# Kernel tuning notes

Measured on AMD Instinct MI355X. Metric: run time of the kernel, lower is better.

Reference implementation:

```python
import jax, jax.numpy as jnp
import numpy as np

B, N, F_IN, D, K, INTER = 64, 512, 128, 128, 32, 256
EPS = 1e-5


def _bn(x, g, b, axes):
    # BatchNorm in training mode (biased batch statistics), matching torch BN forward
    m = x.mean(axis=axes, keepdims=True)
    v = x.var(axis=axes, keepdims=True)
    return (x - m) * jax.lax.rsqrt(v + EPS) * g + b


def setup_inputs() -> dict:
    key = jax.random.key(0)
    ks = jax.random.split(key, 12)
    u = lambda k, s: jax.random.uniform(k, s, jnp.float32, -0.3, 0.3)
    return {
        "data": jax.random.normal(ks[0], (B, N, F_IN), jnp.float32),
        "emb_weight": u(ks[1], (N, D)),          # nn.Embedding(node_num, dim), kaiming-uniform-ish
        "lin_W": u(ks[2], (F_IN, D)),            # GraphLayer lin (no bias)
        "att_i": u(ks[3], (D,)),
        "att_j": u(ks[4], (D,)),
        "att_em_i": u(ks[5], (D,)),
        "att_em_j": u(ks[6], (D,)),
        "gnn_bias": jnp.zeros((D,), jnp.float32),
        "gnn_bn_g": jnp.ones((D,), jnp.float32),
        "gnn_bn_b": jnp.zeros((D,), jnp.float32),
        "bn_out_g": jnp.ones((D,), jnp.float32),
        "bn_out_b": jnp.zeros((D,), jnp.float32),
        "W1": u(ks[7], (D, INTER)), "b1": jnp.zeros((INTER,), jnp.float32),
        "bn1_g": jnp.ones((INTER,), jnp.float32), "bn1_b": jnp.zeros((INTER,), jnp.float32),
        "W2": u(ks[8], (INTER, INTER)), "b2": jnp.zeros((INTER,), jnp.float32),
        "bn2_g": jnp.ones((INTER,), jnp.float32), "bn2_b": jnp.zeros((INTER,), jnp.float32),
        "W3": u(ks[9], (INTER, 1)), "b3": jnp.zeros((1,), jnp.float32),
    }


def reference(data, emb_weight, lin_W, att_i, att_j, att_em_i, att_em_j,
              gnn_bias, gnn_bn_g, gnn_bn_b, bn_out_g, bn_out_b,
              W1, b1, bn1_g, bn1_b, W2, b2, bn2_g, bn2_b, W3, b3):
    M = B * N
    x = data.reshape(M, F_IN)

    # --- learned graph: cosine similarity + topk over DETACHED embeddings ---
    w = jax.lax.stop_gradient(emb_weight)
    nrm = jnp.linalg.norm(w, axis=-1)
    cos = (w @ w.T) / (nrm[:, None] * nrm[None, :])
    topk_idx = jax.lax.top_k(cos, K)[1]                    # [N, K]

    # gated_edge_index = (j=topk neighbor as source, i as target), tiled per batch
    src0 = topk_idx.reshape(-1)                            # [N*K] sources (j)
    dst0 = jnp.repeat(jnp.arange(N), K)                    # [N*K] targets (i)
    off = (jnp.arange(B) * N)[:, None]
    src = (src0[None, :] + off).reshape(-1)                # [B*N*K]
    dst = (dst0[None, :] + off).reshape(-1)
    valid = src != dst                                     # remove_self_loops
    loops = jnp.arange(M)                                  # add_self_loops
    src = jnp.concatenate([src, loops])
    dst = jnp.concatenate([dst, loops])
    valid = jnp.concatenate([valid, jnp.ones((M,), bool)])

    # --- GraphLayer (GAT-style, heads=1, concat=False) ---
    x_lin = x @ lin_W                                      # [M, D]
    emb_b = jnp.tile(emb_weight, (B, 1))                   # [M, D] embedding repeated per batch
    # per-node score halves; gather scalars at edges instead of [E, 2D] keys
    s_i = x_lin @ att_i + emb_b @ att_em_i                 # key_i . cat(att_i, att_em_i)
    s_j = x_lin @ att_j + emb_b @ att_em_j
    logit = jax.nn.leaky_relu(s_i[dst] + s_j[src], 0.2)    # [E]
    logit = jnp.where(valid, logit, -1e9)                  # removed self-edges contribute 0
    mx = jax.ops.segment_max(logit, dst, num_segments=M)
    e = jnp.where(valid, jnp.exp(logit - mx[dst]), 0.0)
    den = jax.ops.segment_sum(e, dst, num_segments=M)
    alpha = e / den[dst]                                   # softmax over incoming edges
    agg = jax.ops.segment_sum(x_lin[src] * alpha[:, None], dst, num_segments=M)
    gcn = jax.nn.relu(_bn(agg + gnn_bias, gnn_bn_g, gnn_bn_b, (0,)))  # GNNLayer bn+relu

    # --- gating by embedding, BN over channel dim, OutLayer MLP ---
    h = gcn.reshape(B, N, D) * emb_weight[None]            # [B, N, D]
    h = jax.nn.relu(_bn(h, bn_out_g, bn_out_b, (0, 1)))    # BatchNorm1d over D channels
    # dropout p=0.2 is identity in eval mode
    o = jax.nn.relu(_bn(h @ W1 + b1, bn1_g, bn1_b, (0, 1)))
    o = jax.nn.relu(_bn(o @ W2 + b2, bn2_g, bn2_b, (0, 1)))
    o = (o @ W3 + b3).reshape(B, N)                        # out.view(-1, node_num)
    return o
```

## Files before the change

### kernel.cpp

```cpp
#include <hip/hip_runtime.h>
#include <math.h>

#define M_ROWS 32768
#define NNODES 512
#define KNBR   32
#define EPSBN  1e-5f

typedef __bf16 bf16x8 __attribute__((ext_vector_type(8)));
typedef __bf16 bf16x4 __attribute__((ext_vector_type(4)));
typedef __bf16 bf16x2 __attribute__((ext_vector_type(2)));
typedef float  f32x4  __attribute__((ext_vector_type(4)));

#if defined(__has_builtin)
#if __has_builtin(__builtin_amdgcn_global_load_lds)
#define HAVE_GLL 1
#endif
#endif

__device__ __forceinline__ void async_ld16(void* lds, const void* g){
#ifdef HAVE_GLL
    __builtin_amdgcn_global_load_lds((__attribute__((address_space(1))) void*)(g),
                                     (__attribute__((address_space(3))) void*)(lds),
                                     16, 0, 0);
#else
    *(bf16x8*)lds = *(const bf16x8*)g;
#endif
}

__global__ __launch_bounds__(256) void k1_kernel(
    const float* __restrict__ data, const float* __restrict__ emb,
    const float* __restrict__ lin_W, const float* __restrict__ W1,
    const float* __restrict__ W2,
    const float* __restrict__ att_i, const float* __restrict__ att_j,
    const float* __restrict__ aem_i, const float* __restrict__ aem_j,
    int* __restrict__ topk, float* __restrict__ e_i, float* __restrict__ e_j,
    __bf16* __restrict__ Wp1, __bf16* __restrict__ Wp2,
    float* __restrict__ stats,
    __bf16* __restrict__ xlin, float* __restrict__ s_i, float* __restrict__ s_j)
{
    __shared__ __align__(16) char sm[50176];
    int bid = blockIdx.x, tid = threadIdx.x;

    if (bid < 512){
        __bf16 (*As)[136] = (__bf16(*)[136])sm;
        bf16x8* Bp = (bf16x8*)(sm + 17408);
        int lane = tid & 63, wv = tid >> 6;
        int mrow = lane & 15, q = lane >> 4;
        int row0 = bid * 64;

        #pragma unroll
        for (int i = 0; i < 8; ++i){
            int g = tid + i*256;
            int kg = g >> 7, c = g & 127;
            bf16x8 pk;
            #pragma unroll
            for (int j = 0; j < 8; ++j) pk[j] = (__bf16)lin_W[(size_t)(kg*8 + j)*128 + c];
            Bp[g] = pk;
        }
        #pragma unroll
        for (int i = 0; i < 4; ++i){
            int p = tid + i*256;
            int r = p >> 4, c8 = p & 15;
            const float* src = &data[(size_t)(row0 + r)*128 + c8*8];
            float4 a0 = *(const float4*)src;
            float4 a1 = *(const float4*)(src + 4);
            bf16x8 o;
            o[0]=(__bf16)a0.x; o[1]=(__bf16)a0.y; o[2]=(__bf16)a0.z; o[3]=(__bf16)a0.w;
            o[4]=(__bf16)a1.x; o[5]=(__bf16)a1.y; o[6]=(__bf16)a1.z; o[7]=(__bf16)a1.w;
            *(bf16x8*)&As[r][c8*8] = o;
        }
        __syncthreads();

        f32x4 acc[8];
        #pragma unroll
        for (int ct = 0; ct < 8; ++ct) acc[ct] = (f32x4){0.f,0.f,0.f,0.f};
        #pragma unroll
        for (int ks = 0; ks < 4; ++ks){
            bf16x8 a = *(const bf16x8*)&As[wv*16 + mrow][ks*32 + q*8];
            #pragma unroll
            for (int ct = 0; ct < 8; ++ct){
                bf16x8 bb = Bp[(ks*4 + q)*128 + ct*16 + mrow];
                acc[ct] = __builtin_amdgcn_mfma_f32_16x16x32_bf16(a, bb, acc[ct], 0, 0, 0);
            }
        }

        float ai[4] = {0,0,0,0}, aj[4] = {0,0,0,0};
        #pragma unroll
        for (int ct = 0; ct < 8; ++ct){
            int col = ct*16 + mrow;
            float wti = att_i[col], wtj = att_j[col];
            #pragma unroll
            for (int reg = 0; reg < 4; ++reg){
                int row = row0 + wv*16 + q*4 + reg;
                float v = acc[ct][reg];
                xlin[(size_t)row*128 + col] = (__bf16)v;
                ai[reg] += v*wti; aj[reg] += v*wtj;
            }
        }
        #pragma unroll
        for (int mask = 1; mask < 16; mask <<= 1){
            #pragma unroll
            for (int reg = 0; reg < 4; ++reg){
                ai[reg] += __shfl_xor(ai[reg], mask);
                aj[reg] += __shfl_xor(aj[reg], mask);
            }
        }
        if (mrow == 0){
            #pragma unroll
            for (int reg = 0; reg < 4; ++reg){
                int row = row0 + wv*16 + q*4 + reg;
                s_i[row] = ai[reg];
                s_j[row] = aj[reg];
            }
        }
        return;
    }

    if (bid >= 1024){
        if (bid == 1072){
            for (int i = tid; i < 1536; i += 256) stats[i] = 0.f;
            return;
        }
        int gidx = (bid - 1024)*256 + tid;
        const float* W; __bf16* o; int lg;
        if (gidx < 4096){ W = W1; o = Wp1; lg = gidx; }
        else            { W = W2; o = Wp2; lg = gidx - 4096; }
        int kg = lg >> 8, c = lg & 255;
        bf16x8 pk;
        #pragma unroll
        for (int j = 0; j < 8; ++j) pk[j] = (__bf16)W[(size_t)(kg*8 + j)*256 + c];
        *(bf16x8*)&o[(size_t)lg*8] = pk;
        return;
    }

    float* wi   = (float*)sm;
    float* sval = (float*)(sm + 512);
    int*   sidx = (int*)(sm + 2560);
    int row = bid - 512;
    if (tid < 128) wi[tid] = emb[row*128 + tid];
    __syncthreads();

    if (tid >= 64 && tid < 128){
        int lane = tid - 64;
        float ai = wi[lane]*aem_i[lane] + wi[lane+64]*aem_i[lane+64];
        float aj = wi[lane]*aem_j[lane] + wi[lane+64]*aem_j[lane+64];
        #pragma unroll
        for (int off = 32; off; off >>= 1){
            ai += __shfl_down(ai, off);
            aj += __shfl_down(aj, off);
        }
        if (lane == 0){ e_i[row] = ai; e_j[row] = aj; }
    }

    float ni = 0.f;
    #pragma unroll 8
    for (int d = 0; d < 128; ++d) ni += wi[d]*wi[d];
    float rni = sqrtf(ni);
    for (int jj = tid; jj < 512; jj += 256){
        const float4* wj4 = (const float4*)(emb + jj*128);
        float dot = 0.f, nj = 0.f;
        #pragma unroll 8
        for (int d4 = 0; d4 < 32; ++d4){
            float4 w = wj4[d4];
            dot += wi[4*d4+0]*w.x + wi[4*d4+1]*w.y + wi[4*d4+2]*w.z + wi[4*d4+3]*w.w;
            nj  += w.x*w.x + w.y*w.y + w.z*w.z + w.w*w.w;
        }
        sval[jj] = dot / (rni * sqrtf(nj));
        sidx[jj] = jj;
    }
    __syncthreads();

    #pragma unroll 1
    for (int k = 2; k <= 512; k <<= 1){
        #pragma unroll 1
        for (int j = k >> 1; j > 0; j >>= 1){
            int i2 = ((tid & ~(j-1)) << 1) | (tid & (j-1));
            int p  = i2 | j;
            float vi = sval[i2], vp = sval[p];
            int   xi = sidx[i2], xp = sidx[p];
            bool i_before_p = (vi > vp) || (vi == vp && xi < xp);
            bool up = ((i2 & k) == 0);
            if (up ? !i_before_p : i_before_p){
                sval[i2] = vp; sval[p] = vi;
                sidx[i2] = xp; sidx[p] = xi;
            }
            __syncthreads();
        }
    }
    if (tid < KNBR) topk[row*KNBR + tid] = sidx[tid];
}

__global__ __launch_bounds__(256) void agg_kernel(const __bf16* __restrict__ xl,
                                                  const float* __restrict__ s_i,
                                                  const float* __restrict__ s_j,
                                                  const float* __restrict__ e_i,
                                                  const float* __restrict__ e_j,
                                                  const int* __restrict__ topk,
                                                  const float2* __restrict__ gnn_bias2,
                                                  __bf16* __restrict__ aggp){
    int tid = threadIdx.x;
    int wv = tid >> 6, lane = tid & 63;
    int blk = blockIdx.x;
    int xcd = blk & 7, grp = blk >> 3;
    int batch = xcd*8 + (grp >> 7);
    int node  = (grp & 127)*4 + wv;
    int m = batch*512 + node;
    int i = node;

    int src; bool valid;
    if (lane < KNBR){ int j = topk[i*KNBR + lane]; src = batch*512 + j; valid = (j != i); }
    else            { src = m; valid = (lane == KNBR); }
    float l = s_i[m] + e_i[i] + s_j[src] + e_j[src & 511];
    l = (l >= 0.f) ? l : 0.2f*l;
    l = valid ? l : -1e30f;
    float mx = l;
    #pragma unroll
    for (int mask = 1; mask < 64; mask <<= 1) mx = fmaxf(mx, __shfl_xor(mx, mask));
    float e = valid ? __expf(l - mx) : 0.f;
    float den = e;
    #pragma unroll
    for (int mask = 1; mask < 64; mask <<= 1) den += __shfl_xor(den, mask);
    float alpha = e / den;

    float2 acc = make_float2(0.f, 0.f);
    #pragma unroll 4
    for (int k = 0; k < 33; ++k){
        float a = __shfl(alpha, k);
        int   s = __shfl(src, k);
        bf16x2 v = *(const bf16x2*)&xl[(size_t)s*128 + lane*2];
        acc.x += a*(float)v[0]; acc.y += a*(float)v[1];
    }
    float2 bv = gnn_bias2[lane];
    bf16x2 o;
    o[0] = (__bf16)(acc.x + bv.x);
    o[1] = (__bf16)(acc.y + bv.y);
    *(bf16x2*)&aggp[(size_t)m*128 + lane*2] = o;
}

__global__ __launch_bounds__(256) void colstats_kernel(const __bf16* __restrict__ X,
                                                       float* __restrict__ st){
    int tid = threadIdx.x;
    int cg = tid & 31, rs = tid >> 5;
    int c0 = cg*4;
    float s[4] = {0,0,0,0}, qq[4] = {0,0,0,0};
    for (int m = blockIdx.x*8 + rs; m < M_ROWS; m += gridDim.x*8){
        bf16x4 v = *(const bf16x4*)&X[(size_t)m*128 + c0];
        #pragma unroll
        for (int j = 0; j < 4; ++j){ float f = (float)v[j]; s[j] += f; qq[j] += f*f; }
    }
    __shared__ float rS[8][128], rQ[8][128];
    #pragma unroll
    for (int j = 0; j < 4; ++j){ rS[rs][c0+j] = s[j]; rQ[rs][c0+j] = qq[j]; }
    __syncthreads();
    if (tid < 128){
        float ts = 0.f, tq = 0.f;
        #pragma unroll
        for (int u = 0; u < 8; ++u){ ts += rS[u][tid]; tq += rQ[u][tid]; }
        atomicAdd(&st[tid],       ts);
        atomicAdd(&st[128 + tid], tq);
    }
}

__global__ __launch_bounds__(256) void hstats_kernel(const __bf16* __restrict__ agg,
                                                     const float* __restrict__ gst,
                                                     const float* __restrict__ g,
                                                     const float* __restrict__ bta,
                                                     const float* __restrict__ emb,
                                                     float* __restrict__ hstats){
    int tid = threadIdx.x;
    int cg = tid & 31, rs = tid >> 5;
    int c0 = cg*4;
    float sc[4], sh[4];
    #pragma unroll
    for (int j = 0; j < 4; ++j){
        float mean = gst[c0+j] * (1.f/32768.f);
        float var  = gst[128 + c0+j] * (1.f/32768.f) - mean*mean;
        sc[j] = g[c0+j] / sqrtf(var + EPSBN);
        sh[j] = bta[c0+j] - mean*sc[j];
    }
    float s[4] = {0,0,0,0}, qq[4] = {0,0,0,0};
    for (int m = blockIdx.x*8 + rs; m < M_ROWS; m += gridDim.x*8){
        bf16x4 v = *(const bf16x4*)&agg[(size_t)m*128 + c0];
        float4 e = *(const float4*)&emb[(size_t)(m & 511)*128 + c0];
        float f0 = fmaxf((float)v[0]*sc[0] + sh[0], 0.f) * e.x;
        float f1 = fmaxf((float)v[1]*sc[1] + sh[1], 0.f) * e.y;
        float f2 = fmaxf((float)v[2]*sc[2] + sh[2], 0.f) * e.z;
        float f3 = fmaxf((float)v[3]*sc[3] + sh[3], 0.f) * e.w;
        s[0]+=f0; qq[0]+=f0*f0; s[1]+=f1; qq[1]+=f1*f1;
        s[2]+=f2; qq[2]+=f2*f2; s[3]+=f3; qq[3]+=f3*f3;
    }
    __shared__ float rS[8][128], rQ[8][128];
    #pragma unroll
    for (int j = 0; j < 4; ++j){ rS[rs][c0+j] = s[j]; rQ[rs][c0+j] = qq[j]; }
    __syncthreads();
    if (tid < 128){
        float ts = 0.f, tq = 0.f;
        #pragma unroll
        for (int u = 0; u < 8; ++u){ ts += rS[u][tid]; tq += rQ[u][tid]; }
        atomicAdd(&hstats[tid],       ts);
        atomicAdd(&hstats[128 + tid], tq);
    }
}

template<bool GATE>
__global__ __launch_bounds__(256) void gemm2_kernel(
    const __bf16* __restrict__ A, int a_stride, int Ktot,
    const float* __restrict__ st1, const float* __restrict__ g1, const float* __restrict__ b1,
    const float* __restrict__ emb,
    const float* __restrict__ st2, const float* __restrict__ g2, const float* __restrict__ b2,
    const __bf16* __restrict__ Wp, int Ctot,
    const float* __restrict__ bias,
    __bf16* __restrict__ outp,
    float* __restrict__ outstats, int outK)
{
    __shared__ __align__(16) __bf16 As[128][136];
    __shared__ __align__(16) __bf16 Bp[16][128][8];
    __shared__ float nsc1[128], nsh1[128], nsc2[128], nsh2[128];
    __shared__ float statS[128], statQ[128];

    int tid  = threadIdx.x;
    int lane = tid & 63, wv = tid >> 6;
    int mrow = lane & 15, q = lane >> 4;
    int wvr = wv & 1, wvc = wv >> 1;
    int cb0  = blockIdx.y * 128;
    int row0 = blockIdx.x * 128;

    f32x4 acc[4][4];
    #pragma unroll
    for (int rt = 0; rt < 4; ++rt)
        #pragma unroll
        for (int ct = 0; ct < 4; ++ct)
            acc[rt][ct] = (f32x4){0.f,0.f,0.f,0.f};

    for (int kc = 0; kc < Ktot; kc += 128){
        if (tid < 128){
            int f = kc + tid;
            float mean = st1[f] * (1.f/32768.f);
            float var  = st1[Ktot + f] * (1.f/32768.f) - mean*mean;
            float sc   = g1[f] / sqrtf(var + EPSBN);
            nsc1[tid] = sc;
            nsh1[tid] = b1[f] - mean*sc;
            if (GATE){
                float mean2 = st2[tid] * (1.f/32768.f);
                float var2  = st2[128 + tid] * (1.f/32768.f) - mean2*mean2;
                float sc2   = g2[tid] / sqrtf(var2 + EPSBN);
                nsc2[tid] = sc2;
                nsh2[tid] = b2[tid] - mean2*sc2;
            }
        }
        __syncthreads();

        int kg0 = kc >> 3;
        #pragma unroll
        for (int i = 0; i < 8; ++i){
            int p = tid + i*256;
            const __bf16* src = Wp + ((size_t)(kg0 + (p>>7))*Ctot + cb0 + (p&127))*8;
            async_ld16((__bf16*)Bp + (size_t)p*8, src);
        }
        #pragma unroll
        for (int i = 0; i < 8; ++i){
            int p = tid + i*256;
            int r = p >> 4, c8 = p & 15;
            bf16x8 v = *(const bf16x8*)&A[(size_t)(row0 + r)*a_stride + kc + c8*8];
            bf16x8 o;
            if (GATE){
                const float* ep = &emb[(size_t)((row0 + r) & 511)*128 + c8*8];
                float4 e0 = *(const float4*)ep;
                float4 e1 = *(const float4*)(ep + 4);
                float ee[8] = {e0.x,e0.y,e0.z,e0.w,e1.x,e1.y,e1.z,e1.w};
                #pragma unroll
                for (int j = 0; j < 8; ++j){
                    int f = c8*8 + j;
                    float hv = fmaxf((float)v[j]*nsc1[f] + nsh1[f], 0.f) * ee[j];
                    o[j] = (__bf16)fmaxf(hv*nsc2[f] + nsh2[f], 0.f);
                }
            } else {
                #pragma unroll
                for (int j = 0; j < 8; ++j){
                    int f = c8*8 + j;
                    o[j] = (__bf16)fmaxf((float)v[j]*nsc1[f] + nsh1[f], 0.f);
                }
            }
            *(bf16x8*)&As[r][c8*8] = o;
        }
        __syncthreads();

        #pragma unroll
        for (int ks = 0; ks < 4; ++ks){
            bf16x8 a[4];
            #pragma unroll
            for (int rt = 0; rt < 4; ++rt)
                a[rt] = *(const bf16x8*)&As[wvr*64 + rt*16 + mrow][ks*32 + q*8];
            #pragma unroll
            for (int ct = 0; ct < 4; ++ct){
                bf16x8 bb = *(const bf16x8*)&Bp[ks*4 + q][wvc*64 + ct*16 + mrow][0];
                #pragma unroll
                for (int rt = 0; rt < 4; ++rt)
                    acc[rt][ct] = __builtin_amdgcn_mfma_f32_16x16x32_bf16(a[rt], bb, acc[rt][ct], 0, 0, 0);
            }
        }
        __syncthreads();
    }

    if (tid < 128){ statS[tid] = 0.f; statQ[tid] = 0.f; }
    __syncthreads();

    float cs[4] = {0,0,0,0}, cq[4] = {0,0,0,0};
    #pragma unroll
    for (int ct = 0; ct < 4; ++ct){
        int lcol = wvc*64 + ct*16 + mrow;
        int col  = cb0 + lcol;
        float bvv = bias[col];
        #pragma unroll
        for (int rt = 0; rt < 4; ++rt){
            #pragma unroll
            for (int reg = 0; reg < 4; ++reg){
                int row = row0 + wvr*64 + rt*16 + q*4 + reg;
                __bf16 ov = (__bf16)(acc[rt][ct][reg] + bvv);
                outp[(size_t)row*Ctot + col] = ov;
                float fv = (float)ov; cs[ct] += fv; cq[ct] += fv*fv;
            }
        }
    }
    #pragma unroll
    for (int ct = 0; ct < 4; ++ct){
        float s  = cs[ct]; s  += __shfl_xor(s, 16);  s  += __shfl_xor(s, 32);
        float qq = cq[ct]; qq += __shfl_xor(qq, 16); qq += __shfl_xor(qq, 32);
        if (q == 0){
            atomicAdd(&statS[wvc*64 + ct*16 + mrow], s);
            atomicAdd(&statQ[wvc*64 + ct*16 + mrow], qq);
        }
    }
    __syncthreads();
    if (tid < 128){
        atomicAdd(&outstats[cb0 + tid],        statS[tid]);
        atomicAdd(&outstats[outK + cb0 + tid], statQ[tid]);
    }
}

__global__ __launch_bounds__(256) void final_kernel(const __bf16* __restrict__ t2,
                                                    const float* __restrict__ st,
                                                    const float* __restrict__ g,
                                                    const float* __restrict__ bta,
                                                    const float* __restrict__ W3,
                                                    const float* __restrict__ b3,
                                                    float* __restrict__ outp){
    int gid = blockIdx.x*256 + threadIdx.x;
    int wid = gid >> 6, lane = gid & 63;
    int c0 = lane*4;
    bf16x4 v  = *(const bf16x4*)&t2[(size_t)wid*256 + c0];
    float4 w3 = *(const float4*)&W3[c0];
    float4 gg = *(const float4*)&g[c0];
    float4 bb = *(const float4*)&bta[c0];
    float4 sm = *(const float4*)&st[c0];
    float4 sq = *(const float4*)&st[256 + c0];
    float accv = 0.f;
    {
        float mean, var, val;
        mean = sm.x*(1.f/32768.f); var = sq.x*(1.f/32768.f) - mean*mean;
        val = ((float)v[0]-mean)*(gg.x/sqrtf(var+EPSBN)) + bb.x; accv += fmaxf(val,0.f)*w3.x;
        mean = sm.y*(1.f/32768.f); var = sq.y*(1.f/32768.f) - mean*mean;
        val = ((float)v[1]-mean)*(gg.y/sqrtf(var+EPSBN)) + bb.y; accv += fmaxf(val,0.f)*w3.y;
        mean = sm.z*(1.f/32768.f); var = sq.z*(1.f/32768.f) - mean*mean;
        val = ((float)v[2]-mean)*(gg.z/sqrtf(var+EPSBN)) + bb.z; accv += fmaxf(val,0.f)*w3.z;
        mean = sm.w*(1.f/32768.f); var = sq.w*(1.f/32768.f) - mean*mean;
        val = ((float)v[3]-mean)*(gg.w/sqrtf(var+EPSBN)) + bb.w; accv += fmaxf(val,0.f)*w3.w;
    }
    for (int off = 32; off; off >>= 1) accv += __shfl_down(accv, off);
    if (lane == 0) outp[wid] = accv + b3[0];
}

extern "C" void kernel_launch(void* const* d_in, const int* in_sizes, int n_in,
                              void* d_out, int out_size, void* d_ws, size_t ws_size,
                              hipStream_t stream)
{
    (void)in_sizes; (void)n_in; (void)out_size; (void)ws_size;
    const float* data   = (const float*)d_in[0];
    const float* emb    = (const float*)d_in[1];
    const float* lin_W  = (const float*)d_in[2];
    const float* att_i  = (const float*)d_in[3];
    const float* att_j  = (const float*)d_in[4];
    const float* aem_i  = (const float*)d_in[5];
    const float* aem_j  = (const float*)d_in[6];
    const float* gnn_bias = (const float*)d_in[7];
    const float* gnn_g  = (const float*)d_in[8];
    const float* gnn_b  = (const float*)d_in[9];
    const float* bno_g  = (const float*)d_in[10];
    const float* bno_b  = (const float*)d_in[11];
    const float* W1     = (const float*)d_in[12];
    const float* b1     = (const float*)d_in[13];
    const float* bn1_g  = (const float*)d_in[14];
    const float* bn1_b  = (const float*)d_in[15];
    const float* W2     = (const float*)d_in[16];
    const float* b2     = (const float*)d_in[17];
    const float* bn2_g  = (const float*)d_in[18];
    const float* bn2_b  = (const float*)d_in[19];
    const float* W3     = (const float*)d_in[20];
    const float* b3     = (const float*)d_in[21];
    float* outp = (float*)d_out;
    char*  ws   = (char*)d_ws;

    int*    topk     = (int*)ws;
    float*  e_i      = (float*)(ws + 65536);
    float*  e_j      = (float*)(ws + 67584);
    float*  s_i      = (float*)(ws + 69632);
    float*  s_j      = (float*)(ws + 200704);
    float*  stats    = (float*)(ws + 331776);
    float*  gnnstats = stats;
    float*  hstats   = stats + 256;
    float*  bn1stats = stats + 512;
    float*  bn2stats = stats + 1024;
    __bf16* Wp1      = (__bf16*)(ws + 337920);
    __bf16* Wp2      = (__bf16*)(ws + 403456);
    __bf16* xlin     = (__bf16*)(ws + 1048576);
    __bf16* aggb     = (__bf16*)(ws + 1048576 +   8388608);
    __bf16* t1       = (__bf16*)(ws + 1048576 + 2*8388608);
    __bf16* t2       = (__bf16*)(ws + 1048576 + 2*8388608 + 16777216);

    k1_kernel<<<1073, 256, 0, stream>>>(data, emb, lin_W, W1, W2, att_i, att_j,
                                        aem_i, aem_j, topk, e_i, e_j,
                                        Wp1, Wp2, stats, xlin, s_i, s_j);

    agg_kernel<<<8192, 256, 0, stream>>>(xlin, s_i, s_j, e_i, e_j, topk,
                                         (const float2*)gnn_bias, aggb);

    colstats_kernel<<<256, 256, 0, stream>>>(aggb, gnnstats);
    hstats_kernel<<<256, 256, 0, stream>>>(aggb, gnnstats, gnn_g, gnn_b, emb, hstats);

    gemm2_kernel<true><<<dim3(256,2), 256, 0, stream>>>(
        aggb, 128, 128, gnnstats, gnn_g, gnn_b, emb, hstats, bno_g, bno_b,
        Wp1, 256, b1, t1, bn1stats, 256);

    gemm2_kernel<false><<<dim3(256,2), 256, 0, stream>>>(
        t1, 256, 256, bn1stats, bn1_g, bn1_b, nullptr, nullptr, nullptr, nullptr,
        Wp2, 256, b2, t2, bn2stats, 256);

    final_kernel<<<M_ROWS/4, 256, 0, stream>>>(t2, bn2stats, bn2_g, bn2_b, W3, b3, outp);
}
```

Measured before the change: 246.6 us.

## Fuse GNN column statistics into aggregation kernel with sliced partial atomics

```diff
diff --git a/kernel.cpp b/kernel.cpp
--- a/kernel.cpp
+++ b/kernel.cpp
@@ -35,7 +35,7 @@
     const float* __restrict__ aem_i, const float* __restrict__ aem_j,
     int* __restrict__ topk, float* __restrict__ e_i, float* __restrict__ e_j,
     __bf16* __restrict__ Wp1, __bf16* __restrict__ Wp2,
-    float* __restrict__ stats,
+    float* __restrict__ stats, float* __restrict__ gnnpart,
     __bf16* __restrict__ xlin, float* __restrict__ s_i, float* __restrict__ s_j)
 {
     __shared__ __align__(16) char sm[50176];
@@ -119,6 +119,7 @@
     if (bid >= 1024){
         if (bid == 1072){
             for (int i = tid; i < 1536; i += 256) stats[i] = 0.f;
+            for (int i = tid; i < 16384; i += 256) gnnpart[i] = 0.f;
             return;
         }
         int gidx = (bid - 1024)*256 + tid;
@@ -197,7 +198,8 @@
                                                   const float* __restrict__ e_j,
                                                   const int* __restrict__ topk,
                                                   const float2* __restrict__ gnn_bias2,
-                                                  __bf16* __restrict__ aggp){
+                                                  __bf16* __restrict__ aggp,
+                                                  float* __restrict__ gnnpart){
     int tid = threadIdx.x;
     int wv = tid >> 6, lane = tid & 63;
     int blk = blockIdx.x;
@@ -222,59 +224,64 @@
     for (int mask = 1; mask < 64; mask <<= 1) den += __shfl_xor(den, mask);
     float alpha = e / den;
 
-    float2 acc = make_float2(0.f, 0.f);
-    #pragma unroll 4
+    float ak[33]; int sk[33];
+    #pragma unroll
     for (int k = 0; k < 33; ++k){
-        float a = __shfl(alpha, k);
-        int   s = __shfl(src, k);
-        bf16x2 v = *(const bf16x2*)&xl[(size_t)s*128 + lane*2];
-        acc.x += a*(float)v[0]; acc.y += a*(float)v[1];
+        ak[k] = __shfl(alpha, k);
+        sk[k] = __shfl(src, k);
+    }
+    float ax0 = 0.f, ay0 = 0.f, ax1 = 0.f, ay1 = 0.f;
+    #pragma unroll
+    for (int k = 0; k < 33; ++k){
+        bf16x2 v = *(const bf16x2*)&xl[(size_t)sk[k]*128 + lane*2];
+        if (k & 1){ ax1 += ak[k]*(float)v[0]; ay1 += ak[k]*(float)v[1]; }
+        else      { ax0 += ak[k]*(float)v[0]; ay0 += ak[k]*(float)v[1]; }
     }
     float2 bv = gnn_bias2[lane];
     bf16x2 o;
-    o[0] = (__bf16)(acc.x + bv.x);
-    o[1] = (__bf16)(acc.y + bv.y);
+    o[0] = (__bf16)(ax0 + ax1 + bv.x);
+    o[1] = (__bf16)(ay0 + ay1 + bv.y);
     *(bf16x2*)&aggp[(size_t)m*128 + lane*2] = o;
-}
-
-__global__ __launch_bounds__(256) void colstats_kernel(const __bf16* __restrict__ X,
-                                                       float* __restrict__ st){
-    int tid = threadIdx.x;
-    int cg = tid & 31, rs = tid >> 5;
-    int c0 = cg*4;
-    float s[4] = {0,0,0,0}, qq[4] = {0,0,0,0};
-    for (int m = blockIdx.x*8 + rs; m < M_ROWS; m += gridDim.x*8){
-        bf16x4 v = *(const bf16x4*)&X[(size_t)m*128 + c0];
-        #pragma unroll
-        for (int j = 0; j < 4; ++j){ float f = (float)v[j]; s[j] += f; qq[j] += f*f; }
-    }
-    __shared__ float rS[8][128], rQ[8][128];
-    #pragma unroll
-    for (int j = 0; j < 4; ++j){ rS[rs][c0+j] = s[j]; rQ[rs][c0+j] = qq[j]; }
+
+    float r0 = (float)o[0], r1 = (float)o[1];
+    __shared__ float rS[4][128], rQ[4][128];
+    rS[wv][lane*2]   = r0;    rS[wv][lane*2+1] = r1;
+    rQ[wv][lane*2]   = r0*r0; rQ[wv][lane*2+1] = r1*r1;
     __syncthreads();
     if (tid < 128){
-        float ts = 0.f, tq = 0.f;
-        #pragma unroll
-        for (int u = 0; u < 8; ++u){ ts += rS[u][tid]; tq += rQ[u][tid]; }
-        atomicAdd(&st[tid],       ts);
-        atomicAdd(&st[128 + tid], tq);
+        float ts = rS[0][tid] + rS[1][tid] + rS[2][tid] + rS[3][tid];
+        float tq = rQ[0][tid] + rQ[1][tid] + rQ[2][tid] + rQ[3][tid];
+        float* slice = gnnpart + (blk & 63)*256;
+        atomicAdd(&slice[tid],       ts);
+        atomicAdd(&slice[128 + tid], tq);
     }
 }
 
 __global__ __launch_bounds__(256) void hstats_kernel(const __bf16* __restrict__ agg,
-                                                     const float* __restrict__ gst,
+                                                     const float* __restrict__ gnnpart,
+                                                     float* __restrict__ gnnstats,
                                                      const float* __restrict__ g,
                                                      const float* __restrict__ bta,
                                                      const float* __restrict__ emb,
                                                      float* __restrict__ hstats){
+    __shared__ float gred[256];
     int tid = threadIdx.x;
+    {
+        float t = 0.f;
+        #pragma unroll 8
+        for (int s2 = 0; s2 < 64; ++s2) t += gnnpart[s2*256 + tid];
+        gred[tid] = t;
+        if (blockIdx.x == 0) gnnstats[tid] = t;
+    }
+    __syncthreads();
+
     int cg = tid & 31, rs = tid >> 5;
     int c0 = cg*4;
     float sc[4], sh[4];
     #pragma unroll
     for (int j = 0; j < 4; ++j){
-        float mean = gst[c0+j] * (1.f/32768.f);
-        float var  = gst[128 + c0+j] * (1.f/32768.f) - mean*mean;
+        float mean = gred[c0+j] * (1.f/32768.f);
+        float var  = gred[128 + c0+j] * (1.f/32768.f) - mean*mean;
         sc[j] = g[c0+j] / sqrtf(var + EPSBN);
         sh[j] = bta[c0+j] - mean*sc[j];
     }
@@ -512,6 +519,7 @@
     float*  bn2stats = stats + 1024;
     __bf16* Wp1      = (__bf16*)(ws + 337920);
     __bf16* Wp2      = (__bf16*)(ws + 403456);
+    float*  gnnpart  = (float*)(ws + 534528);
     __bf16* xlin     = (__bf16*)(ws + 1048576);
     __bf16* aggb     = (__bf16*)(ws + 1048576 +   8388608);
     __bf16* t1       = (__bf16*)(ws + 1048576 + 2*8388608);
@@ -519,13 +527,13 @@
 
     k1_kernel<<<1073, 256, 0, stream>>>(data, emb, lin_W, W1, W2, att_i, att_j,
                                         aem_i, aem_j, topk, e_i, e_j,
-                                        Wp1, Wp2, stats, xlin, s_i, s_j);
+                                        Wp1, Wp2, stats, gnnpart, xlin, s_i, s_j);
 
     agg_kernel<<<8192, 256, 0, stream>>>(xlin, s_i, s_j, e_i, e_j, topk,
-                                         (const float2*)gnn_bias, aggb);
-
-    colstats_kernel<<<256, 256, 0, stream>>>(aggb, gnnstats);
-    hstats_kernel<<<256, 256, 0, stream>>>(aggb, gnnstats, gnn_g, gnn_b, emb, hstats);
+                                         (const float2*)gnn_bias, aggb, gnnpart);
+
+    hstats_kernel<<<256, 256, 0, stream>>>(aggb, gnnpart, gnnstats,
+                                           gnn_g, gnn_b, emb, hstats);
 
     gemm2_kernel<true><<<dim3(256,2), 256, 0, stream>>>(
         aggb, 128, 128, gnnstats, gnn_g, gnn_b, emb, hstats, bno_g, bno_b,
```

Result: faster. 240.6 us, median of 2 (-2.4%).
